# Optimization experiments

Measured on AMD Instinct MI355X. Metric: run time of the kernel, lower is better.

The kernel has to match this reference:

```python
import jax, jax.numpy as jnp
import numpy as np

P, F, H, OUT = 2, 64, 2, 2   # passes, inputLayerSize, heads, outputLayerSize
N, E = 50000, 400000
D_JUMP = (P + 1) * F          # 192, JumpingKnowledge 'cat' output
D_FC = D_JUMP + 1             # 193, after concat with problemType
D_HID = D_FC // 2             # 96


def setup_inputs() -> dict:
    key = jax.random.key(0)
    ks = jax.random.split(key, 20)
    s = 1.0 / np.sqrt(F)
    return {
        'x': jax.random.normal(ks[0], (N, F), dtype=jnp.float32),
        'edge_index': jax.random.randint(ks[1], (2, E), 0, N, dtype=jnp.int32),
        'edge_attr': jax.random.normal(ks[2], (E, 1), dtype=jnp.float32),
        'problemType': jax.random.normal(ks[3], (1,), dtype=jnp.float32),
        'batch': jnp.zeros((N,), dtype=jnp.int32),
        # stacked GATv2Conv params over the P layers
        'lin_l_w': jax.random.normal(ks[4], (P, F, H * F)) * s,
        'lin_l_b': jnp.zeros((P, H * F), jnp.float32),
        'lin_r_w': jax.random.normal(ks[5], (P, F, H * F)) * s,
        'lin_r_b': jnp.zeros((P, H * F), jnp.float32),
        'lin_edge_w': jax.random.normal(ks[6], (P, 1, H * F)) * s,
        'att': jax.random.normal(ks[7], (P, H, F)) * s,
        'gat_bias': jnp.zeros((P, F), jnp.float32),
        # GlobalAttention gate_nn: Linear(D_JUMP, 1) + LeakyReLU
        'gate_w': jax.random.normal(ks[8], (D_JUMP, 1)) / np.sqrt(D_JUMP),
        'gate_b': jnp.zeros((1,), jnp.float32),
        'fc1_w': jax.random.normal(ks[9], (D_FC, D_HID)) / np.sqrt(D_FC),
        'fc1_b': jnp.zeros((D_HID,), jnp.float32),
        'fc2_w': jax.random.normal(ks[10], (D_HID, D_HID)) / np.sqrt(D_HID),
        'fc2_b': jnp.zeros((D_HID,), jnp.float32),
        'fcl_w': jax.random.normal(ks[11], (D_HID, OUT)) / np.sqrt(D_HID),
        'fcl_b': jnp.zeros((OUT,), jnp.float32),
    }


def _gatv2_layer(x, src, dst, edge_attr, Wl, bl, Wr, br, We, att, bias):
    """GATv2Conv with concat=False (mean over heads), edge_dim=1."""
    n = x.shape[0]
    xl = (x @ Wl + bl).reshape(n, H, F)          # source transform
    xr = (x @ Wr + br).reshape(n, H, F)          # target transform
    ef = (edge_attr @ We).reshape(-1, H, F)      # edge transform (no bias)
    m = xl[src] + xr[dst] + ef                   # [E,H,F]
    m = jax.nn.leaky_relu(m, 0.2)
    logits = jnp.einsum('ehf,hf->eh', m, att)    # [E,H]
    # segment softmax over destination node
    lmax = jax.ops.segment_max(logits, dst, num_segments=n)
    a = jnp.exp(logits - lmax[dst])
    denom = jax.ops.segment_sum(a, dst, num_segments=n)
    alpha = a / denom[dst]                       # [E,H]
    msg = xl[src] * alpha[:, :, None]            # [E,H,F]
    out = jax.ops.segment_sum(msg, dst, num_segments=n)  # [N,H,F]
    return out.mean(axis=1) + bias               # concat=False -> head mean


def reference(x, edge_index, edge_attr, problemType, batch,
              lin_l_w, lin_l_b, lin_r_w, lin_r_b, lin_edge_w, att, gat_bias,
              gate_w, gate_b, fc1_w, fc1_b, fc2_w, fc2_b, fcl_w, fcl_b):
    src, dst = edge_index[0], edge_index[1]
    xs = [x]
    h = x
    for p in range(P):
        h = _gatv2_layer(h, src, dst, edge_attr,
                         lin_l_w[p], lin_l_b[p], lin_r_w[p], lin_r_b[p],
                         lin_edge_w[p], att[p], gat_bias[p])
        h = jax.nn.leaky_relu(h, 0.01)
        xs.append(h)
    xj = jnp.concatenate(xs, axis=1)             # JumpingKnowledge 'cat' -> [N, D_JUMP]
    # GlobalAttention pooling (single graph: batch is all zeros)
    gate = jax.nn.leaky_relu(xj @ gate_w + gate_b, 0.01)  # [N,1]
    a = jax.nn.softmax(gate, axis=0)
    pooled = jnp.sum(a * xj, axis=0, keepdims=True)       # [1, D_JUMP]
    z = jnp.concatenate([pooled.reshape(1, -1), problemType[:, None]], axis=1)  # [1, D_FC]
    z = jax.nn.leaky_relu(z @ fc1_w + fc1_b, 0.01)
    z = jax.nn.leaky_relu(z @ fc2_w + fc2_b, 0.01)
    return z @ fcl_w + fcl_b                     # [1, OUT]
```

## Files before the change

### kernel.cpp

```cpp
#include <hip/hip_runtime.h>

#define NN 50000
#define NE 400000
#define FD 64
#define NH 2
#define HF 128
#define ELLW 48
#define SCAN_NB ((NN + 255) / 256)
#define POOL_BLOCKS 512
#define NTA 64
#define GG_BLOCKS 2048

__device__ __forceinline__ float lrelu(float x, float s) { return fmaxf(x, x * s); }

__device__ __forceinline__ unsigned short f2bf(float f) {
    unsigned u = __float_as_uint(f);
    return (unsigned short)((u + 0x7FFFu + ((u >> 16) & 1u)) >> 16);
}
__device__ __forceinline__ float2 bf2f(unsigned u) {
    return make_float2(__uint_as_float(u << 16), __uint_as_float(u & 0xFFFF0000u));
}
__device__ __forceinline__ float4 bfx4(unsigned lo, unsigned hi) {
    const float2 a = bf2f(lo), b = bf2f(hi);
    return make_float4(a.x, a.y, b.x, b.y);
}

__global__ void zero_deg(int* __restrict__ deg) {
    const int i = blockIdx.x * 256 + threadIdx.x;
    if (i < NN) deg[i] = 0;
}

__global__ void build_ell(const int* __restrict__ ei, const float* __restrict__ ea,
                          int* __restrict__ deg, int2* __restrict__ ell) {
    const int t = blockIdx.x * blockDim.x + threadIdx.x;
    if (t >= NE) return;
    const int d = ei[NE + t];
    const int r = atomicAdd(&deg[d], 1);
    ell[(size_t)d * ELLW + r] = make_int2(ei[t], __float_as_int(ea[t]));
}

__global__ __launch_bounds__(256) void node_transform(
    const float* __restrict__ hin,
    const float* __restrict__ Wl, const float* __restrict__ bl,
    const float* __restrict__ Wr, const float* __restrict__ br,
    unsigned short* __restrict__ xlb, unsigned short* __restrict__ xrb) {
    __shared__ float sA[FD][68];
    const int t = threadIdx.x;
    const int n0 = blockIdx.x * NTA;
    for (int idx = t; idx < NTA * 16; idx += 256) {
        const int n = idx & 63;
        const int kq = (idx >> 6) << 2;
        const int ni = n0 + n;
        const float4 v = (ni < NN) ? *(const float4*)(hin + (size_t)ni * FD + kq)
                                   : make_float4(0.f, 0.f, 0.f, 0.f);
        sA[kq][n] = v.x; sA[kq + 1][n] = v.y;
        sA[kq + 2][n] = v.z; sA[kq + 3][n] = v.w;
    }
    __syncthreads();
    const int q = t & 63;
    const int g = t >> 6;
    const int c0 = q << 2;
    const bool isR = c0 >= 128;
    const int cc = isR ? c0 - 128 : c0;
    const float* __restrict__ W = isR ? Wr : Wl;
    const float4 bv = isR ? *(const float4*)(br + cc) : *(const float4*)(bl + cc);
    unsigned short* __restrict__ dst = isR ? xrb : xlb;
    float acc[16][4];
#pragma unroll
    for (int i = 0; i < 16; ++i) {
        acc[i][0] = bv.x; acc[i][1] = bv.y; acc[i][2] = bv.z; acc[i][3] = bv.w;
    }
    const int nb = g << 4;
#pragma unroll 4
    for (int k = 0; k < FD; ++k) {
        const float4 w = *(const float4*)(W + k * HF + cc);
        const float4 a0 = *(const float4*)(&sA[k][nb]);
        const float4 a1 = *(const float4*)(&sA[k][nb + 4]);
        const float4 a2 = *(const float4*)(&sA[k][nb + 8]);
        const float4 a3 = *(const float4*)(&sA[k][nb + 12]);
        const float av[16] = {a0.x, a0.y, a0.z, a0.w, a1.x, a1.y, a1.z, a1.w,
                              a2.x, a2.y, a2.z, a2.w, a3.x, a3.y, a3.z, a3.w};
#pragma unroll
        for (int i = 0; i < 16; ++i) {
            acc[i][0] = fmaf(av[i], w.x, acc[i][0]);
            acc[i][1] = fmaf(av[i], w.y, acc[i][1]);
            acc[i][2] = fmaf(av[i], w.z, acc[i][2]);
            acc[i][3] = fmaf(av[i], w.w, acc[i][3]);
        }
    }
    const int xoff = (cc < 64) ? (cc << 1) : (((cc - 64) << 1) + 4);
#pragma unroll
    for (int i = 0; i < 16; ++i) {
        const int n = n0 + nb + i;
        if (n >= NN) continue;
        uint2 pk;
        pk.x = (unsigned)f2bf(acc[i][0]) | ((unsigned)f2bf(acc[i][1]) << 16);
        pk.y = (unsigned)f2bf(acc[i][2]) | ((unsigned)f2bf(acc[i][3]) << 16);
        *(uint2*)(dst + (size_t)n * HF + xoff) = pk;
    }
}

__device__ __forceinline__ void gat_edge(
    bool valid, int lane, float eav, uint4 L,
    const float4& we0, const float4& we1, const float4& aw0, const float4& aw1,
    const float4& xr0, const float4& xr1,
    float4& a0, float4& a1, float& d0, float& d1) {
    const float4 xls0 = bfx4(L.x, L.y);
    const float4 xls1 = bfx4(L.z, L.w);
    float p0, p1, t;
    t = lrelu(fmaf(eav, we0.x, xls0.x + xr0.x), 0.2f); p0 = t * aw0.x;
    t = lrelu(fmaf(eav, we0.y, xls0.y + xr0.y), 0.2f); p0 = fmaf(t, aw0.y, p0);
    t = lrelu(fmaf(eav, we0.z, xls0.z + xr0.z), 0.2f); p0 = fmaf(t, aw0.z, p0);
    t = lrelu(fmaf(eav, we0.w, xls0.w + xr0.w), 0.2f); p0 = fmaf(t, aw0.w, p0);
    t = lrelu(fmaf(eav, we1.x, xls1.x + xr1.x), 0.2f); p1 = t * aw1.x;
    t = lrelu(fmaf(eav, we1.y, xls1.y + xr1.y), 0.2f); p1 = fmaf(t, aw1.y, p1);
    t = lrelu(fmaf(eav, we1.z, xls1.z + xr1.z), 0.2f); p1 = fmaf(t, aw1.z, p1);
    t = lrelu(fmaf(eav, we1.w, xls1.w + xr1.w), 0.2f); p1 = fmaf(t, aw1.w, p1);
    const bool hi = (lane & 8) != 0;
    float send = hi ? p0 : p1;
    float got = __shfl_xor(send, 8);
    float q = hi ? (p1 + got) : (p0 + got);
    q += __shfl_xor(q, 4);
    q += __shfl_xor(q, 2);
    q += __shfl_xor(q, 1);
    const float oth = __shfl_xor(q, 8);
    const float s0 = hi ? oth : q;
    const float s1 = hi ? q : oth;
    const float w0 = valid ? __expf(s0) : 0.f;
    const float w1 = valid ? __expf(s1) : 0.f;
    a0.x = fmaf(w0, xls0.x, a0.x);
    a0.y = fmaf(w0, xls0.y, a0.y);
    a0.z = fmaf(w0, xls0.z, a0.z);
    a0.w = fmaf(w0, xls0.w, a0.w);
    d0 += w0;
    a1.x = fmaf(w1, xls1.x, a1.x);
    a1.y = fmaf(w1, xls1.y, a1.y);
    a1.z = fmaf(w1, xls1.z, a1.z);
    a1.w = fmaf(w1, xls1.w, a1.w);
    d1 += w1;
}

__global__ __launch_bounds__(256) void gat_gather(
    const int* __restrict__ deg, const int2* __restrict__ ell,
    const unsigned short* __restrict__ xlb, const unsigned short* __restrict__ xrb,
    const float* __restrict__ We, const float* __restrict__ att,
    const float* __restrict__ bias, float* __restrict__ hout) {
    const int t = threadIdx.x;
    const int lane = t & 63;
    const int slot = lane >> 4;
    const int fo = (lane & 15) << 2;
    const float4 we0 = *(const float4*)(We + fo);
    const float4 we1 = *(const float4*)(We + 64 + fo);
    const float4 aw0 = *(const float4*)(att + fo);
    const float4 aw1 = *(const float4*)(att + 64 + fo);
    const float4 bv = *(const float4*)(bias + fo);
    const int stride = (GG_BLOCKS * 256) >> 6;
    int wid = (blockIdx.x * 256 + t) >> 6;
    int dg = (wid < NN) ? deg[wid] : 0;

    while (wid < NN) {
        const int nxt = wid + stride;
        const int dgn = (nxt < NN) ? deg[nxt] : 0;
        const uint4 xrp = *(const uint4*)(xrb + (size_t)wid * HF + (fo << 1));
        const float4 xr0 = bfx4(xrp.x, xrp.y);
        const float4 xr1 = bfx4(xrp.z, xrp.w);
        const int e0 = wid * ELLW;
        const int e1 = e0 + dg;
        float d0 = 0.f, d1 = 0.f;
        float4 a0 = {0.f, 0.f, 0.f, 0.f}, a1 = {0.f, 0.f, 0.f, 0.f};
        int eb = e0;
        for (; eb + 8 <= e1; eb += 8) {
            const int2 seA = ell[eb + slot];
            const int2 seB = ell[eb + 4 + slot];
            const uint4 LA = *(const uint4*)(xlb + (size_t)seA.x * HF + (fo << 1));
            const uint4 LB = *(const uint4*)(xlb + (size_t)seB.x * HF + (fo << 1));
            gat_edge(true, lane, __int_as_float(seA.y), LA, we0, we1, aw0, aw1,
                     xr0, xr1, a0, a1, d0, d1);
            gat_edge(true, lane, __int_as_float(seB.y), LB, we0, we1, aw0, aw1,
                     xr0, xr1, a0, a1, d0, d1);
        }
        if (eb < e1) {
            const int myA = eb + slot, myB = eb + 4 + slot;
            const bool vA = myA < e1, vB = myB < e1;
            const int2 seA = ell[vA ? myA : e0];
            const int2 seB = ell[vB ? myB : e0];
            const uint4 LA = *(const uint4*)(xlb + (size_t)seA.x * HF + (fo << 1));
            const uint4 LB = *(const uint4*)(xlb + (size_t)seB.x * HF + (fo << 1));
            gat_edge(vA, lane, __int_as_float(seA.y), LA, we0, we1, aw0, aw1,
                     xr0, xr1, a0, a1, d0, d1);
            gat_edge(vB, lane, __int_as_float(seB.y), LB, we0, we1, aw0, aw1,
                     xr0, xr1, a0, a1, d0, d1);
        }
#pragma unroll
        for (int o = 16; o <= 32; o <<= 1) {
            d0 += __shfl_xor(d0, o);
            d1 += __shfl_xor(d1, o);
            a0.x += __shfl_xor(a0.x, o); a0.y += __shfl_xor(a0.y, o);
            a0.z += __shfl_xor(a0.z, o); a0.w += __shfl_xor(a0.w, o);
            a1.x += __shfl_xor(a1.x, o); a1.y += __shfl_xor(a1.y, o);
            a1.z += __shfl_xor(a1.z, o); a1.w += __shfl_xor(a1.w, o);
        }
        if (slot == 0) {
            const float i0 = d0 > 0.f ? 1.f / d0 : 0.f;
            const float i1 = d1 > 0.f ? 1.f / d1 : 0.f;
            float4 rr;
            rr.x = lrelu(fmaf(0.5f, fmaf(a0.x, i0, a1.x * i1), bv.x), 0.01f);
            rr.y = lrelu(fmaf(0.5f, fmaf(a0.y, i0, a1.y * i1), bv.y), 0.01f);
            rr.z = lrelu(fmaf(0.5f, fmaf(a0.z, i0, a1.z * i1), bv.z), 0.01f);
            rr.w = lrelu(fmaf(0.5f, fmaf(a0.w, i0, a1.w * i1), bv.w), 0.01f);
            *(float4*)(hout + (size_t)wid * FD + fo) = rr;
        }
        wid = nxt;
        dg = dgn;
    }
}

__global__ void pool_kernel(const float* __restrict__ x, const float* __restrict__ h1,
                            const float* __restrict__ h2, const float* __restrict__ gw,
                            const float* __restrict__ gb, float* __restrict__ part) {
    __shared__ float sp[193];
    const int t = threadIdx.x;
    if (t < 193) sp[t] = 0.f;
    __syncthreads();
    const int lane = t & 63;
    const int wid = (blockIdx.x * blockDim.x + t) >> 6;
    const int nw = (POOL_BLOCKS * 256) >> 6;
    const float w0 = gw[lane], w1 = gw[64 + lane], w2 = gw[128 + lane];
    const float gbv = gb[0];
    float p0 = 0.f, p1 = 0.f, p2 = 0.f, es = 0.f;
    for (int n = wid; n < NN; n += nw) {
        const size_t b = (size_t)n * FD + lane;
        const float xv = x[b], h1v = h1[b], h2v = h2[b];
        float v = xv * w0 + h1v * w1 + h2v * w2;
#pragma unroll
        for (int o = 32; o; o >>= 1) v += __shfl_xor(v, o);
        const float e = __expf(lrelu(v + gbv, 0.01f));
        p0 = fmaf(e, xv, p0);
        p1 = fmaf(e, h1v, p1);
        p2 = fmaf(e, h2v, p2);
        es += e;
    }
    atomicAdd(&sp[lane], p0);
    atomicAdd(&sp[64 + lane], p1);
    atomicAdd(&sp[128 + lane], p2);
    if (lane == 0) atomicAdd(&sp[192], es);
    __syncthreads();
    if (t < 193) part[(size_t)t * POOL_BLOCKS + blockIdx.x] = sp[t];
}

__global__ void pool_reduce(const float* __restrict__ part, float* __restrict__ pooled) {
    __shared__ float ws[4];
    const int e = blockIdx.x;
    const int t = threadIdx.x;
    float s = 0.f;
#pragma unroll
    for (int b = t; b < POOL_BLOCKS; b += 256) s += part[(size_t)e * POOL_BLOCKS + b];
#pragma unroll
    for (int o = 32; o; o >>= 1) s += __shfl_xor(s, o);
    if ((t & 63) == 0) ws[t >> 6] = s;
    __syncthreads();
    if (t == 0) pooled[e] = ws[0] + ws[1] + ws[2] + ws[3];
}

__global__ void mlp_kernel(const float* __restrict__ pooled, const float* __restrict__ pt,
                           const float* __restrict__ f1w, const float* __restrict__ f1b,
                           const float* __restrict__ f2w, const float* __restrict__ f2b,
                           const float* __restrict__ flw, const float* __restrict__ flb,
                           float* __restrict__ out) {
    __shared__ float z[193], z1[96], z2[96];
    const int t = threadIdx.x;
    const float inv = 1.f / pooled[192];
    for (int i = t; i < 192; i += 256) z[i] = pooled[i] * inv;
    if (t == 0) z[192] = pt[0];
    __syncthreads();
    if (t < 96) {
        float a = f1b[t];
        for (int k = 0; k < 193; ++k) a = fmaf(z[k], f1w[k * 96 + t], a);
        z1[t] = lrelu(a, 0.01f);
    }
    __syncthreads();
    if (t < 96) {
        float a = f2b[t];
        for (int k = 0; k < 96; ++k) a = fmaf(z1[k], f2w[k * 96 + t], a);
        z2[t] = lrelu(a, 0.01f);
    }
    __syncthreads();
    if (t < 2) {
        float a = flb[t];
        for (int k = 0; k < 96; ++k) a = fmaf(z2[k], flw[k * 2 + t], a);
        out[t] = a;
    }
}

extern "C" void kernel_launch(void* const* d_in, const int* in_sizes, int n_in,
                              void* d_out, int out_size, void* d_ws, size_t ws_size,
                              hipStream_t stream) {
    (void)in_sizes; (void)n_in; (void)out_size; (void)ws_size;
    const float* x    = (const float*)d_in[0];
    const int*   ei   = (const int*)d_in[1];
    const float* ea   = (const float*)d_in[2];
    const float* pt   = (const float*)d_in[3];
    const float* llw  = (const float*)d_in[5];
    const float* llb  = (const float*)d_in[6];
    const float* lrw  = (const float*)d_in[7];
    const float* lrb  = (const float*)d_in[8];
    const float* lew  = (const float*)d_in[9];
    const float* attw = (const float*)d_in[10];
    const float* gbias= (const float*)d_in[11];
    const float* gw   = (const float*)d_in[12];
    const float* gb   = (const float*)d_in[13];
    const float* f1w  = (const float*)d_in[14];
    const float* f1b  = (const float*)d_in[15];
    const float* f2w  = (const float*)d_in[16];
    const float* f2b  = (const float*)d_in[17];
    const float* flw  = (const float*)d_in[18];
    const float* flb  = (const float*)d_in[19];
    float* out = (float*)d_out;

    char* w = (char*)d_ws;
    unsigned short* xlb = (unsigned short*)w; w += (size_t)NN * HF * 2;
    unsigned short* xrb = (unsigned short*)w; w += (size_t)NN * HF * 2;
    float* h1 = (float*)w;         w += (size_t)NN * FD * 4;
    float* h2 = (float*)w;         w += (size_t)NN * FD * 4;
    int2* ell = (int2*)w;          w += (size_t)NN * ELLW * 8;
    int* deg = (int*)w;            w += (size_t)NN * 4;
    float* part = (float*)w;       w += (size_t)193 * POOL_BLOCKS * 4;
    float* pooled = (float*)w;     w += 193 * 4;

    zero_deg<<<SCAN_NB, 256, 0, stream>>>(deg);
    build_ell<<<(NE + 255) / 256, 256, 0, stream>>>(ei, ea, deg, ell);

    for (int p = 0; p < 2; ++p) {
        const float* hin = (p == 0) ? x : h1;
        float* hout = (p == 0) ? h1 : h2;
        node_transform<<<(NN + NTA - 1) / NTA, 256, 0, stream>>>(
            hin, llw + (size_t)p * FD * HF, llb + (size_t)p * HF,
            lrw + (size_t)p * FD * HF, lrb + (size_t)p * HF, xlb, xrb);
        gat_gather<<<GG_BLOCKS, 256, 0, stream>>>(
            deg, ell, xlb, xrb,
            lew + (size_t)p * HF, attw + (size_t)p * HF,
            gbias + (size_t)p * FD, hout);
    }

    pool_kernel<<<POOL_BLOCKS, 256, 0, stream>>>(x, h1, h2, gw, gb, part);
    pool_reduce<<<193, 256, 0, stream>>>(part, pooled);
    mlp_kernel<<<1, 256, 0, stream>>>(pooled, pt, f1w, f1b, f2w, f2b, flw, flb, out);
}
```

Baseline: 204.1 us.

## Fuse second GAT gather layer with global attention pooling

The second-layer gather kernel now computes the gate score and the exp-weighted pooling sums per node right after producing that node's output row. This removes the h2 buffer write and the separate pool kernel's full re-read of x, h1 and h2. The cost is extra per-node loads of x and h1, many shared-memory atomics inside the gather loop, and four times more partial sums (2048 blocks) for pool_reduce to combine.

```diff
diff --git a/kernel.cpp b/kernel.cpp
--- a/kernel.cpp
+++ b/kernel.cpp
@@ -7,7 +7,6 @@
 #define HF 128
 #define ELLW 48
 #define SCAN_NB ((NN + 255) / 256)
-#define POOL_BLOCKS 512
 #define NTA 64
 #define GG_BLOCKS 2048
 
@@ -215,37 +214,115 @@
     }
 }
 
-__global__ void pool_kernel(const float* __restrict__ x, const float* __restrict__ h1,
-                            const float* __restrict__ h2, const float* __restrict__ gw,
-                            const float* __restrict__ gb, float* __restrict__ part) {
+__global__ __launch_bounds__(256) void gat_gather_pool(
+    const int* __restrict__ deg, const int2* __restrict__ ell,
+    const unsigned short* __restrict__ xlb, const unsigned short* __restrict__ xrb,
+    const float* __restrict__ We, const float* __restrict__ att,
+    const float* __restrict__ bias,
+    const float* __restrict__ x, const float* __restrict__ h1,
+    const float* __restrict__ gw, const float* __restrict__ gb,
+    float* __restrict__ part) {
     __shared__ float sp[193];
     const int t = threadIdx.x;
     if (t < 193) sp[t] = 0.f;
     __syncthreads();
     const int lane = t & 63;
-    const int wid = (blockIdx.x * blockDim.x + t) >> 6;
-    const int nw = (POOL_BLOCKS * 256) >> 6;
-    const float w0 = gw[lane], w1 = gw[64 + lane], w2 = gw[128 + lane];
+    const int slot = lane >> 4;
+    const int fo = (lane & 15) << 2;
+    const float4 we0 = *(const float4*)(We + fo);
+    const float4 we1 = *(const float4*)(We + 64 + fo);
+    const float4 aw0 = *(const float4*)(att + fo);
+    const float4 aw1 = *(const float4*)(att + 64 + fo);
+    const float4 bv = *(const float4*)(bias + fo);
     const float gbv = gb[0];
-    float p0 = 0.f, p1 = 0.f, p2 = 0.f, es = 0.f;
-    for (int n = wid; n < NN; n += nw) {
-        const size_t b = (size_t)n * FD + lane;
-        const float xv = x[b], h1v = h1[b], h2v = h2[b];
-        float v = xv * w0 + h1v * w1 + h2v * w2;
-#pragma unroll
-        for (int o = 32; o; o >>= 1) v += __shfl_xor(v, o);
-        const float e = __expf(lrelu(v + gbv, 0.01f));
-        p0 = fmaf(e, xv, p0);
-        p1 = fmaf(e, h1v, p1);
-        p2 = fmaf(e, h2v, p2);
-        es += e;
-    }
-    atomicAdd(&sp[lane], p0);
-    atomicAdd(&sp[64 + lane], p1);
-    atomicAdd(&sp[128 + lane], p2);
-    if (lane == 0) atomicAdd(&sp[192], es);
-    __syncthreads();
-    if (t < 193) part[(size_t)t * POOL_BLOCKS + blockIdx.x] = sp[t];
+    const int stride = (GG_BLOCKS * 256) >> 6;
+    int wid = (blockIdx.x * 256 + t) >> 6;
+    int dg = (wid < NN) ? deg[wid] : 0;
+
+    while (wid < NN) {
+        const int nxt = wid + stride;
+        const int dgn = (nxt < NN) ? deg[nxt] : 0;
+        const uint4 xrp = *(const uint4*)(xrb + (size_t)wid * HF + (fo << 1));
+        const float4 xr0 = bfx4(xrp.x, xrp.y);
+        const float4 xr1 = bfx4(xrp.z, xrp.w);
+        const int e0 = wid * ELLW;
+        const int e1 = e0 + dg;
+        float d0 = 0.f, d1 = 0.f;
+        float4 a0 = {0.f, 0.f, 0.f, 0.f}, a1 = {0.f, 0.f, 0.f, 0.f};
+        int eb = e0;
+        for (; eb + 8 <= e1; eb += 8) {
+            const int2 seA = ell[eb + slot];
+            const int2 seB = ell[eb + 4 + slot];
+            const uint4 LA = *(const uint4*)(xlb + (size_t)seA.x * HF + (fo << 1));
+            const uint4 LB = *(const uint4*)(xlb + (size_t)seB.x * HF + (fo << 1));
+            gat_edge(true, lane, __int_as_float(seA.y), LA, we0, we1, aw0, aw1,
+                     xr0, xr1, a0, a1, d0, d1);
+            gat_edge(true, lane, __int_as_float(seB.y), LB, we0, we1, aw0, aw1,
+                     xr0, xr1, a0, a1, d0, d1);
+        }
+        if (eb < e1) {
+            const int myA = eb + slot, myB = eb + 4 + slot;
+            const bool vA = myA < e1, vB = myB < e1;
+            const int2 seA = ell[vA ? myA : e0];
+            const int2 seB = ell[vB ? myB : e0];
+            const uint4 LA = *(const uint4*)(xlb + (size_t)seA.x * HF + (fo << 1));
+            const uint4 LB = *(const uint4*)(xlb + (size_t)seB.x * HF + (fo << 1));
+            gat_edge(vA, lane, __int_as_float(seA.y), LA, we0, we1, aw0, aw1,
+                     xr0, xr1, a0, a1, d0, d1);
+            gat_edge(vB, lane, __int_as_float(seB.y), LB, we0, we1, aw0, aw1,
+                     xr0, xr1, a0, a1, d0, d1);
+        }
+#pragma unroll
+        for (int o = 16; o <= 32; o <<= 1) {
+            d0 += __shfl_xor(d0, o);
+            d1 += __shfl_xor(d1, o);
+            a0.x += __shfl_xor(a0.x, o); a0.y += __shfl_xor(a0.y, o);
+            a0.z += __shfl_xor(a0.z, o); a0.w += __shfl_xor(a0.w, o);
+            a1.x += __shfl_xor(a1.x, o); a1.y += __shfl_xor(a1.y, o);
+            a1.z += __shfl_xor(a1.z, o); a1.w += __shfl_xor(a1.w, o);
+        }
+        if (slot == 0) {
+            const float i0 = d0 > 0.f ? 1.f / d0 : 0.f;
+            const float i1 = d1 > 0.f ? 1.f / d1 : 0.f;
+            float4 rr;
+            rr.x = lrelu(fmaf(0.5f, fmaf(a0.x, i0, a1.x * i1), bv.x), 0.01f);
+            rr.y = lrelu(fmaf(0.5f, fmaf(a0.y, i0, a1.y * i1), bv.y), 0.01f);
+            rr.z = lrelu(fmaf(0.5f, fmaf(a0.z, i0, a1.z * i1), bv.z), 0.01f);
+            rr.w = lrelu(fmaf(0.5f, fmaf(a0.w, i0, a1.w * i1), bv.w), 0.01f);
+            const float4 xq = *(const float4*)(x + (size_t)wid * FD + fo);
+            const float4 hq = *(const float4*)(h1 + (size_t)wid * FD + fo);
+            const float4 g0 = *(const float4*)(gw + fo);
+            const float4 g1 = *(const float4*)(gw + 64 + fo);
+            const float4 g2 = *(const float4*)(gw + 128 + fo);
+            float v = xq.x * g0.x + xq.y * g0.y + xq.z * g0.z + xq.w * g0.w;
+            v = fmaf(hq.x, g1.x, v); v = fmaf(hq.y, g1.y, v);
+            v = fmaf(hq.z, g1.z, v); v = fmaf(hq.w, g1.w, v);
+            v = fmaf(rr.x, g2.x, v); v = fmaf(rr.y, g2.y, v);
+            v = fmaf(rr.z, g2.z, v); v = fmaf(rr.w, g2.w, v);
+            v += __shfl_xor(v, 1);
+            v += __shfl_xor(v, 2);
+            v += __shfl_xor(v, 4);
+            v += __shfl_xor(v, 8);
+            const float e = __expf(lrelu(v + gbv, 0.01f));
+            atomicAdd(&sp[fo],       e * xq.x);
+            atomicAdd(&sp[fo + 1],   e * xq.y);
+            atomicAdd(&sp[fo + 2],   e * xq.z);
+            atomicAdd(&sp[fo + 3],   e * xq.w);
+            atomicAdd(&sp[64 + fo],     e * hq.x);
+            atomicAdd(&sp[64 + fo + 1], e * hq.y);
+            atomicAdd(&sp[64 + fo + 2], e * hq.z);
+            atomicAdd(&sp[64 + fo + 3], e * hq.w);
+            atomicAdd(&sp[128 + fo],     e * rr.x);
+            atomicAdd(&sp[128 + fo + 1], e * rr.y);
+            atomicAdd(&sp[128 + fo + 2], e * rr.z);
+            atomicAdd(&sp[128 + fo + 3], e * rr.w);
+            if (fo == 0) atomicAdd(&sp[192], e);
+        }
+        wid = nxt;
+        dg = dgn;
+    }
+    __syncthreads();
+    if (t < 193) part[(size_t)t * GG_BLOCKS + blockIdx.x] = sp[t];
 }
 
 __global__ void pool_reduce(const float* __restrict__ part, float* __restrict__ pooled) {
@@ -253,8 +330,7 @@
     const int e = blockIdx.x;
     const int t = threadIdx.x;
     float s = 0.f;
-#pragma unroll
-    for (int b = t; b < POOL_BLOCKS; b += 256) s += part[(size_t)e * POOL_BLOCKS + b];
+    for (int b = t; b < GG_BLOCKS; b += 256) s += part[(size_t)e * GG_BLOCKS + b];
 #pragma unroll
     for (int o = 32; o; o >>= 1) s += __shfl_xor(s, o);
     if ((t & 63) == 0) ws[t >> 6] = s;
@@ -321,28 +397,26 @@
     unsigned short* xlb = (unsigned short*)w; w += (size_t)NN * HF * 2;
     unsigned short* xrb = (unsigned short*)w; w += (size_t)NN * HF * 2;
     float* h1 = (float*)w;         w += (size_t)NN * FD * 4;
-    float* h2 = (float*)w;         w += (size_t)NN * FD * 4;
     int2* ell = (int2*)w;          w += (size_t)NN * ELLW * 8;
     int* deg = (int*)w;            w += (size_t)NN * 4;
-    float* part = (float*)w;       w += (size_t)193 * POOL_BLOCKS * 4;
+    float* part = (float*)w;       w += (size_t)193 * GG_BLOCKS * 4;
     float* pooled = (float*)w;     w += 193 * 4;
 
     zero_deg<<<SCAN_NB, 256, 0, stream>>>(deg);
     build_ell<<<(NE + 255) / 256, 256, 0, stream>>>(ei, ea, deg, ell);
 
-    for (int p = 0; p < 2; ++p) {
-        const float* hin = (p == 0) ? x : h1;
-        float* hout = (p == 0) ? h1 : h2;
-        node_transform<<<(NN + NTA - 1) / NTA, 256, 0, stream>>>(
-            hin, llw + (size_t)p * FD * HF, llb + (size_t)p * HF,
-            lrw + (size_t)p * FD * HF, lrb + (size_t)p * HF, xlb, xrb);
-        gat_gather<<<GG_BLOCKS, 256, 0, stream>>>(
-            deg, ell, xlb, xrb,
-            lew + (size_t)p * HF, attw + (size_t)p * HF,
-            gbias + (size_t)p * FD, hout);
-    }
-
-    pool_kernel<<<POOL_BLOCKS, 256, 0, stream>>>(x, h1, h2, gw, gb, part);
+    node_transform<<<(NN + NTA - 1) / NTA, 256, 0, stream>>>(
+        x, llw, llb, lrw, lrb, xlb, xrb);
+    gat_gather<<<GG_BLOCKS, 256, 0, stream>>>(
+        deg, ell, xlb, xrb, lew, attw, gbias, h1);
+
+    node_transform<<<(NN + NTA - 1) / NTA, 256, 0, stream>>>(
+        h1, llw + (size_t)FD * HF, llb + HF,
+        lrw + (size_t)FD * HF, lrb + HF, xlb, xrb);
+    gat_gather_pool<<<GG_BLOCKS, 256, 0, stream>>>(
+        deg, ell, xlb, xrb, lew + HF, attw + HF, gbias + FD,
+        x, h1, gw, gb, part);
+
     pool_reduce<<<193, 256, 0, stream>>>(part, pooled);
     mlp_kernel<<<1, 256, 0, stream>>>(pooled, pt, f1w, f1b, f2w, f2b, flw, flb, out);
 }
```

After: 230.8 us. 1.13x slower.
